# Kernel optimization log

Hardware: AMD Instinct MI355X
Metric: run time of the kernel (lower is better)

## Reference

```python
import jax, jax.numpy as jnp
import numpy as np

B, S, D = 2, 1024, 4096
HQ, HKV, HD = 32, 8, 128
GROUPS = HQ // HKV          # 4
SCALE = HD ** -0.5


def _rope_tables(key):
    # standard RoPE cos/sin tables, non-interleaved (half-split) layout
    inv_freq = 1.0 / (10000.0 ** (jnp.arange(0, HD, 2, dtype=jnp.float32) / HD))  # [HD/2]
    pos = jnp.arange(S, dtype=jnp.float32)                                        # [S]
    freqs = pos[:, None] * inv_freq[None, :]                                      # [S, HD/2]
    emb = jnp.concatenate([freqs, freqs], axis=-1)                                # [S, HD]
    cos = jnp.broadcast_to(jnp.cos(emb)[None], (B, S, HD))
    sin = jnp.broadcast_to(jnp.sin(emb)[None], (B, S, HD))
    return cos, sin


def setup_inputs() -> dict:
    key = jax.random.key(0)
    ks = jax.random.split(key, 6)
    hidden_states = jax.random.normal(ks[0], (B, S, D), dtype=jnp.float32)
    cos_table, sin_table = _rope_tables(ks[1])
    Wq = jax.random.normal(ks[2], (D, HQ * HD), dtype=jnp.float32) * (D ** -0.5)
    Wk = jax.random.normal(ks[3], (D, HKV * HD), dtype=jnp.float32) * (D ** -0.5)
    Wv = jax.random.normal(ks[4], (D, HKV * HD), dtype=jnp.float32) * (D ** -0.5)
    Wo = jax.random.normal(ks[5], (HQ * HD, D), dtype=jnp.float32) * ((HQ * HD) ** -0.5)
    return {"hidden_states": hidden_states, "cos_table": cos_table,
            "sin_table": sin_table, "Wq": Wq, "Wk": Wk, "Wv": Wv, "Wo": Wo}


def _rotate_half(x):
    x1, x2 = jnp.split(x, 2, axis=-1)
    return jnp.concatenate([-x2, x1], axis=-1)


def _apply_rope(x, cos, sin):
    # x: [B, S, H, HD]; cos/sin: [B, S, HD] broadcast across heads
    c = cos[:, :, None, :]
    s = sin[:, :, None, :]
    return x * c + _rotate_half(x) * s


def reference(hidden_states, cos_table, sin_table, Wq, Wk, Wv, Wo):
    b, s, _ = hidden_states.shape
    # QKV projections (no bias, Llama-style)
    q = (hidden_states @ Wq).reshape(b, s, HQ, HD)
    k = (hidden_states @ Wk).reshape(b, s, HKV, HD)
    v = (hidden_states @ Wv).reshape(b, s, HKV, HD)
    # fused RoPE on q and k (in [B, S, H, HD] layout, as in source)
    q = _apply_rope(q, cos_table, sin_table)
    k = _apply_rope(k, cos_table, sin_table)
    # -> [B, H, S, HD]
    q = q.transpose(0, 2, 1, 3)
    k = k.transpose(0, 2, 1, 3)
    v = v.transpose(0, 2, 1, 3)
    # GQA repeat_kv: [B, HKV, S, HD] -> [B, HQ, S, HD]
    k = jnp.repeat(k, GROUPS, axis=1)
    v = jnp.repeat(v, GROUPS, axis=1)
    # SDPA, no mask (source calls sdpa without a mask)
    scores = jnp.einsum('bhqd,bhkd->bhqk', q, k) * SCALE
    attn = jax.nn.softmax(scores, axis=-1)
    out = jnp.einsum('bhqk,bhkd->bhqd', attn, v)
    out = out.transpose(0, 2, 1, 3).reshape(b, s, HQ * HD)
    return out @ Wo
```

## Files before the change

### kernel.cpp

```cpp
#include <hip/hip_runtime.h>

#define B_   2
#define S_   1024
#define D_   4096
#define HQ_  32
#define HKV_ 8
#define HD_  128
#define SCALE_ 0.08838834764831845f

typedef unsigned short u16;
typedef __attribute__((ext_vector_type(8))) short s16x8;
typedef __attribute__((ext_vector_type(4))) short s16x4;
typedef __attribute__((ext_vector_type(4))) float f32x4;

#define MFMA(a,b,c) __builtin_amdgcn_mfma_f32_16x16x32_bf16((a),(b),(c),0,0,0)

__device__ __forceinline__ u16 bf16_rne(float x) {
  unsigned u = __float_as_uint(x);
  u += 0x7fffu + ((u >> 16) & 1u);
  return (u16)(u >> 16);
}
__device__ __forceinline__ float bf16_up(u16 h) {
  return __uint_as_float(((unsigned)h) << 16);
}
__device__ __forceinline__ void split2(float x, u16& h, u16& l) {
  h = bf16_rne(x);
  l = bf16_rne(x - bf16_up(h));
}

__device__ __forceinline__ void cvt_hi_lo(float a, float b, unsigned& hi, unsigned& lo) {
  unsigned h, l;
  asm("v_cvt_pk_bf16_f32 %0, %1, %2" : "=v"(h) : "v"(a), "v"(b));
  float ra = __uint_as_float(h << 16);
  float rb = __uint_as_float(h & 0xffff0000u);
  float la = a - ra, lb = b - rb;
  asm("v_cvt_pk_bf16_f32 %0, %1, %2" : "=v"(l) : "v"(la), "v"(lb));
  hi = h; lo = l;
}
__device__ __forceinline__ void pack8(float4 x, float4 y, uint4& h, uint4& l) {
  unsigned h0,h1,h2,h3,l0,l1,l2,l3;
  cvt_hi_lo(x.x, x.y, h0, l0);
  cvt_hi_lo(x.z, x.w, h1, l1);
  cvt_hi_lo(y.x, y.y, h2, l2);
  cvt_hi_lo(y.z, y.w, h3, l3);
  h = make_uint4(h0,h1,h2,h3); l = make_uint4(l0,l1,l2,l3);
}

typedef const __attribute__((address_space(1))) void* gas_ptr;
typedef __attribute__((address_space(3))) void* las_ptr;
__device__ __forceinline__ void gload_lds16(const void* g, void* l) {
  __builtin_amdgcn_global_load_lds((gas_ptr)g, (las_ptr)l, 16, 0, 0);
}

__global__ __launch_bounds__(256) void frag_b(
    const float* __restrict__ W, u16* __restrict__ dh, u16* __restrict__ dl,
    int N, int n0, int Nc16)
{
  __shared__ float T[32][68];
  const int kt = blockIdx.x, nbk = blockIdx.y;
  const int tid = threadIdx.x;
#pragma unroll
  for (int rep = 0; rep < 2; ++rep) {
    int idx = tid + rep * 256;
    int row = idx >> 4, c4 = (idx & 15) * 4;
    float4 v = *reinterpret_cast<const float4*>(&W[(size_t)(kt*32 + row) * N + n0 + nbk*64 + c4]);
    *reinterpret_cast<float4*>(&T[row][c4]) = v;
  }
  __syncthreads();
  const size_t base = ((size_t)kt * Nc16 + nbk * 4) * 512;
  int c = tid;
  int nt = c >> 6, l = c & 63, kc = l >> 4, r = l & 15;
  u16 hh[8], ll[8];
#pragma unroll
  for (int j = 0; j < 8; ++j) split2(T[kc*8 + j][nt*16 + r], hh[j], ll[j]);
  *reinterpret_cast<s16x8*>(&dh[base + (size_t)c * 8]) =
    (s16x8){(short)hh[0],(short)hh[1],(short)hh[2],(short)hh[3],
            (short)hh[4],(short)hh[5],(short)hh[6],(short)hh[7]};
  *reinterpret_cast<s16x8*>(&dl[base + (size_t)c * 8]) =
    (s16x8){(short)ll[0],(short)ll[1],(short)ll[2],(short)ll[3],
            (short)ll[4],(short)ll[5],(short)ll[6],(short)ll[7]};
}

__global__ __launch_bounds__(256) void frag_kv(
    const float* __restrict__ kb, const float* __restrict__ vb,
    const float* __restrict__ cosT, const float* __restrict__ sinT,
    u16* __restrict__ KFh, u16* __restrict__ KFl,
    u16* __restrict__ VFh, u16* __restrict__ VFl)
{
  __shared__ float T[32][132];
  const int bid  = blockIdx.x;
  const int isV  = bid >> 9;
  const int bkvh = (bid >> 5) & 15;
  const int chnk = bid & 31;
  const int tid  = threadIdx.x;
  const int b    = bkvh >> 3, kvh = bkvh & 7;

  const float* src = isV ? vb : kb;
  {
    int r0 = tid >> 5, c4 = (tid & 31) * 4;
    float sgn = (c4 < 64) ? -1.f : 1.f;
#pragma unroll
    for (int it = 0; it < 4; ++it) {
      int row = r0 + it * 8;
      int srow = chnk*32 + row;
      const float* rp = &src[(((size_t)(b * S_ + srow)) * HKV_ + kvh) * HD_];
      float4 v = *reinterpret_cast<const float4*>(rp + c4);
      if (!isV) {
        float4 p  = *reinterpret_cast<const float4*>(rp + (c4 ^ 64));
        float4 cc = *reinterpret_cast<const float4*>(&cosT[((size_t)(b*S_ + srow))*HD_ + c4]);
        float4 ss = *reinterpret_cast<const float4*>(&sinT[((size_t)(b*S_ + srow))*HD_ + c4]);
        v.x = v.x*cc.x + sgn*p.x*ss.x;
        v.y = v.y*cc.y + sgn*p.y*ss.y;
        v.z = v.z*cc.z + sgn*p.z*ss.z;
// ... 213 lines not shown
  float inv_l[4];
#pragma unroll
  for (int r = 0; r < 4; ++r) inv_l[r] = 1.f / l_run[r];
#pragma unroll
  for (int df = 0; df < 8; ++df)
#pragma unroll
    for (int r = 0; r < 4; ++r) {
      int row = qt * 128 + wid * 16 + lg * 4 + r;
      ob[((size_t)((b * S_ + row) * HQ_ + h)) * HD_ + df*16 + lr] = acc_o[df][r] * inv_l[r];
    }
}

__global__ __launch_bounds__(512) void gemm_p1(
    const float* __restrict__ X, const float* __restrict__ abp,
    const u16* __restrict__ WF,
    float* __restrict__ qb, float* __restrict__ kb, float* __restrict__ vb,
    float* __restrict__ outp, int mode, int col0)
{
  __shared__ __attribute__((aligned(16))) u16 lds[40960];
  u16* ah0 = lds;
  u16* al0 = lds + 4096;
  u16* ah1 = lds + 8192;
  u16* al1 = lds + 12288;
  u16* bh0 = lds + 16384;
  u16* bh1 = lds + 24576;
  u16* blb = lds + 32768;

  const int id   = blockIdx.x;
  const int cpx  = gridDim.x >> 3;
  const int swz  = (id & 7) * cpx + (id >> 3);

  const float* A; const u16* Bh; const u16* Bl; float* C;
  int ldc, Nc16, mb, nb;
  if (mode == 0) {
    if (swz < 128)      { A=X; Bh=WF;          Bl=WF+8388608;  C=qb; ldc=4096; Nc16=128; mb=swz>>3; nb=swz&7; }
    else if (swz < 192) { int u=swz-128; A=X; Bh=WF+16777216; Bl=WF+20971520; C=kb; ldc=1024; Nc16=64; mb=u>>2; nb=u&3; }
    else                { int u=swz-192; A=X; Bh=WF+25165824; Bl=WF+29360128; C=vb; ldc=1024; Nc16=64; mb=u>>2; nb=u&3; }
  } else if (mode == 1) {
    A=X; Bh=WF; Bl=WF+8388608; C=qb+col0; ldc=4096; Nc16=128; mb=swz>>3; nb=swz&7;
  } else if (mode == 2) {
    if (swz < 64) { A=X; Bh=WF;          Bl=WF+4194304;  C=kb; ldc=1024; Nc16=64; mb=swz>>2; nb=swz&3; }
    else          { int u=swz-64; A=X; Bh=WF+8388608; Bl=WF+12582912; C=vb; ldc=1024; Nc16=64; mb=u>>2; nb=u&3; }
  } else if (mode == 3) {
    A=abp; Bh=WF; Bl=WF+16777216; C=outp; ldc=4096; Nc16=256; mb=swz>>4; nb=swz&15;
  } else if (mode == 4) {
    A=abp; Bh=WF; Bl=WF+8388608; C=outp+col0; ldc=4096; Nc16=128; mb=swz>>3; nb=swz&7;
  } else {
    if (swz < 128)      { A=X; Bh=WF;          Bl=WF+8388608;  C=qb;      ldc=4096; Nc16=128; mb=swz>>3; nb=swz&7; }
    else if (swz < 256) { int u=swz-128; A=X; Bh=WF+16777216; Bl=WF+25165824; C=qb+2048; ldc=4096; Nc16=128; mb=u>>3; nb=u&7; }
    else if (swz < 320) { int u=swz-256; A=X; Bh=WF+33554432; Bl=WF+37748736; C=kb; ldc=1024; Nc16=64; mb=u>>2; nb=u&3; }
    else                { int u=swz-320; A=X; Bh=WF+41943040; Bl=WF+46137344; C=vb; ldc=1024; Nc16=64; mb=u>>2; nb=u&3; }
  }

  const int tid  = threadIdx.x;
  const int lane = tid & 63;
  const int wid  = tid >> 6;
  const int mtb  = (wid >> 2) * 4;
  const int ntb  = (wid & 3) * 4;
  const int loff = lane * 8;
  const int lg   = lane >> 4;
  const int lr_  = lane & 15;
  const int aoff = (lg*16 + ((lr_ + 4*lg) & 15)) * 8;

  const int arow = tid >> 2;
  const int akc  = tid & 3;
  const float* aptr = A + (size_t)(mb*128 + arow) * 4096 + akc*8;
  const int awr = (arow >> 4)*512 + (akc*16 + (((arow & 15) + 4*akc) & 15))*8;

  const size_t bStep = (size_t)Nc16 * 512;
  const u16* pBh = Bh + (size_t)nb*16*512 + loff;
  const u16* pBl = Bl + (size_t)nb*16*512 + loff;

  f32x4 acc[4][4];
#pragma unroll
  for (int i = 0; i < 4; ++i)
#pragma unroll
    for (int j = 0; j < 4; ++j) acc[i][j] = (f32x4){0.f, 0.f, 0.f, 0.f};

  float4 ra0 = *reinterpret_cast<const float4*>(aptr);
// ... 43 lines not shown

    s16x8 b_l[4];
#pragma unroll
    for (int nf = 0; nf < 4; ++nf)
      b_l[nf] = *reinterpret_cast<const s16x8*>(&blb[(ntb+nf)*512 + loff]);
#pragma unroll
    for (int mf = 0; mf < 4; ++mf)
#pragma unroll
      for (int nf = 0; nf < 4; ++nf)
        acc[mf][nf] = MFMA(a_h[mf], b_l[nf], acc[mf][nf]);
    if (kt < 127) {
      uint4 h4, l4; pack8(ra0, ra1, h4, l4);
      *reinterpret_cast<uint4*>(&nAh[awr]) = h4;
      *reinterpret_cast<uint4*>(&nAl[awr]) = l4;
      if (kt < 126) {
        ra0 = *reinterpret_cast<const float4*>(aptr + (kt+2)*32);
        ra1 = *reinterpret_cast<const float4*>(aptr + (kt+2)*32 + 4);
      }
    }
    __syncthreads();
  }

  const int row0 = mb*128 + (wid >> 2) * 64;
  const int nloc = nb*256 + (wid & 3) * 64;
#pragma unroll
  for (int mf = 0; mf < 4; ++mf)
#pragma unroll
    for (int nf = 0; nf < 4; ++nf)
#pragma unroll
      for (int r = 0; r < 4; ++r)
        C[(size_t)(row0 + mf*16 + lg*4 + r) * ldc + nloc + nf*16 + lr_] = acc[mf][nf][r];
}

__device__ __forceinline__ void gemm_core_128x256(
    const float* __restrict__ A, const float* __restrict__ W,
    float* __restrict__ C, int ldw, int m0, int n0)
{
  __shared__ u16 Ah[128][40];
  __shared__ u16 Al[128][40];
  __shared__ u16 Bh[256][40];
  __shared__ u16 Bl[256][40];

  const int tid  = threadIdx.x;
  const int lane = tid & 63;
  const int wid  = tid >> 6;
  const int wm   = (wid >> 2) * 64;
  const int wn   = (wid & 3) * 64;
  const int lr   = lane & 15;
  const int lg   = lane >> 4;

  f32x4 acc[4][4];
#pragma unroll
  for (int i = 0; i < 4; ++i)
#pragma unroll
    for (int j = 0; j < 4; ++j) acc[i][j] = (f32x4){0.f, 0.f, 0.f, 0.f};

  const int ar  = tid >> 3;
  const int ak  = (tid & 7) * 4;
  const int bn  = tid & 255;
  const int bk0 = (tid >> 8) * 16;

  for (int kt = 0; kt < D_ / 32; ++kt) {
    const int k0 = kt * 32;
    __syncthreads();
#pragma unroll
    for (int j = 0; j < 2; ++j) {
      int r = ar + 64 * j;
      float4 v = *reinterpret_cast<const float4*>(&A[(size_t)(m0 + r) * D_ + k0 + ak]);
      u16 h0,h1,h2,h3,l0,l1,l2,l3;
      split2(v.x,h0,l0); split2(v.y,h1,l1); split2(v.z,h2,l2); split2(v.w,h3,l3);
      *reinterpret_cast<s16x4*>(&Ah[r][ak]) = (s16x4){(short)h0,(short)h1,(short)h2,(short)h3};
      *reinterpret_cast<s16x4*>(&Al[r][ak]) = (s16x4){(short)l0,(short)l1,(short)l2,(short)l3};
    }
    {
      const float* wp = W + (size_t)(k0 + bk0) * ldw + (n0 + bn);
#pragma unroll
      for (int q = 0; q < 4; ++q) {
        float v0 = wp[(q*4 + 0) * (size_t)ldw];
        float v1 = wp[(q*4 + 1) * (size_t)ldw];
        float v2 = wp[(q*4 + 2) * (size_t)ldw];
        float v3 = wp[(q*4 + 3) * (size_t)ldw];
        u16 h0,h1,h2,h3,l0,l1,l2,l3;
        split2(v0,h0,l0); split2(v1,h1,l1); split2(v2,h2,l2); split2(v3,h3,l3);
        *reinterpret_cast<s16x4*>(&Bh[bn][bk0 + q*4]) = (s16x4){(short)h0,(short)h1,(short)h2,(short)h3};
        *reinterpret_cast<s16x4*>(&Bl[bn][bk0 + q*4]) = (s16x4){(short)l0,(short)l1,(short)l2,(short)l3};
      }
    }
    __syncthreads();
    s16x8 a_h[4], a_l[4], b_h[4], b_l[4];
#pragma unroll
    for (int mf = 0; mf < 4; ++mf) {
      a_h[mf] = *reinterpret_cast<const s16x8*>(&Ah[wm + mf*16 + lr][lg*8]);
      a_l[mf] = *reinterpret_cast<const s16x8*>(&Al[wm + mf*16 + lr][lg*8]);
    }
#pragma unroll
    for (int nf = 0; nf < 4; ++nf) {
      b_h[nf] = *reinterpret_cast<const s16x8*>(&Bh[wn + nf*16 + lr][lg*8]);
      b_l[nf] = *reinterpret_cast<const s16x8*>(&Bl[wn + nf*16 + lr][lg*8]);
    }
#pragma unroll
    for (int mf = 0; mf < 4; ++mf)
#pragma unroll
      for (int nf = 0; nf < 4; ++nf) {
        acc[mf][nf] = MFMA(a_h[mf], b_h[nf], acc[mf][nf]);
        acc[mf][nf] = MFMA(a_l[mf], b_h[nf], acc[mf][nf]);
        acc[mf][nf] = MFMA(a_h[mf], b_l[nf], acc[mf][nf]);
      }
  }
#pragma unroll
  for (int mf = 0; mf < 4; ++mf)
#pragma unroll
    for (int nf = 0; nf < 4; ++nf)
#pragma unroll
      for (int r = 0; r < 4; ++r) {
        int row = m0 + wm + mf*16 + lg*4 + r;
        int col = n0 + wn + nf*16 + lr;
        C[(size_t)row * ldw + col] = acc[mf][nf][r];
      }
}

__global__ __launch_bounds__(512) void gemm_qkv_kernel(
    const float* __restrict__ X,
    const float* __restrict__ Wq, const float* __restrict__ Wk,
    const float* __restrict__ Wv,
    float* __restrict__ qb, float* __restrict__ kb, float* __restrict__ vb)
{
  int nbv = blockIdx.x;
  int m0 = blockIdx.y * 128;
  const float* W; float* C; int ldw, n0;
  if (nbv < 16)      { W = Wq; C = qb; ldw = HQ_*HD_;  n0 = nbv * 256; }
  else if (nbv < 20) { W = Wk; C = kb; ldw = HKV_*HD_; n0 = (nbv-16) * 256; }
  else               { W = Wv; C = vb; ldw = HKV_*HD_; n0 = (nbv-20) * 256; }
  gemm_core_128x256(X, W, C, ldw, m0, n0);
}

__global__ __launch_bounds__(512) void gemm_out_kernel(
    const float* __restrict__ A, const float* __restrict__ Wo, float* __restrict__ out)
{
  gemm_core_128x256(A, Wo, out, D_, blockIdx.y * 128, blockIdx.x * 256);
}

__global__ __launch_bounds__(256) void rope_kernel(
    float* __restrict__ qb, float* __restrict__ kb,
    const float* __restrict__ cosT, const float* __restrict__ sinT)
{
  int idx = blockIdx.x * 256 + threadIdx.x;
  const int nq = B_ * S_ * HQ_ * (HD_/2);
  const int nk = B_ * S_ * HKV_ * (HD_/2);
  if (idx < nq) {
    int j = idx & 63;
    int h = (idx >> 6) & (HQ_ - 1);
    int bs = idx >> 11;
    float* p = qb + ((size_t)bs * HQ_ + h) * HD_;
    const float* cp = cosT + (size_t)bs * HD_;
    const float* sp = sinT + (size_t)bs * HD_;
    float x1 = p[j], x2 = p[j + 64];
    p[j]      = x1 * cp[j]      - x2 * sp[j];
    p[j + 64] = x2 * cp[j + 64] + x1 * sp[j + 64];
  } else if (idx < nq + nk) {
    int t2 = idx - nq;
    int j = t2 & 63;
    int h = (t2 >> 6) & (HKV_ - 1);
    int bs = t2 >> 9;
    float* p = kb + ((size_t)bs * HKV_ + h) * HD_;
    const float* cp = cosT + (size_t)bs * HD_;
    const float* sp = sinT + (size_t)bs * HD_;
    float x1 = p[j], x2 = p[j + 64];
    p[j]      = x1 * cp[j]      - x2 * sp[j];
    p[j + 64] = x2 * cp[j + 64] + x1 * sp[j + 64];
  }
}

__global__ __launch_bounds__(512) void attn_kernel(
    const float* __restrict__ qb, const float* __restrict__ kb,
    const float* __restrict__ vb, float* __restrict__ ob)
{
  __shared__ u16 Kh[64][136], Kl[64][136];
  __shared__ u16 Vh[128][72], Vl[128][72];
  __shared__ u16 Ph[8][16][72], Pl[8][16][72];

  const int tid  = threadIdx.x;
  const int lane = tid & 63;
  const int wid  = tid >> 6;
  const int lr   = lane & 15;
  const int lg   = lane >> 4;
  const int qt   = blockIdx.x;
  const int bh   = blockIdx.y;
  const int b    = bh >> 5, h = bh & 31, kvh = h >> 2;

  s16x8 qh[4], ql[4];
  {
    const int qrow = qt * 128 + wid * 16 + lr;
    const float* qp = qb + ((size_t)((b * S_ + qrow) * HQ_ + h)) * HD_;
#pragma unroll
    for (int kc = 0; kc < 4; ++kc) {
      const float* qp2 = qp + kc * 32 + lg * 8;
      float4 v0 = *reinterpret_cast<const float4*>(qp2);
      float4 v1 = *reinterpret_cast<const float4*>(qp2 + 4);
      u16 hh[8], ll[8];
      split2(v0.x,hh[0],ll[0]); split2(v0.y,hh[1],ll[1]);
      split2(v0.z,hh[2],ll[2]); split2(v0.w,hh[3],ll[3]);
      split2(v1.x,hh[4],ll[4]); split2(v1.y,hh[5],ll[5]);
      split2(v1.z,hh[6],ll[6]); split2(v1.w,hh[7],ll[7]);
      qh[kc] = (s16x8){(short)hh[0],(short)hh[1],(short)hh[2],(short)hh[3],
                       (short)hh[4],(short)hh[5],(short)hh[6],(short)hh[7]};
      ql[kc] = (s16x8){(short)ll[0],(short)ll[1],(short)ll[2],(short)ll[3],
                       (short)ll[4],(short)ll[5],(short)ll[6],(short)ll[7]};
    }
  }

  f32x4 acc_o[8];
#pragma unroll
  for (int df = 0; df < 8; ++df) acc_o[df] = (f32x4){0.f, 0.f, 0.f, 0.f};
  float m_run[4] = {-1e30f, -1e30f, -1e30f, -1e30f};
  float l_run[4] = {0.f, 0.f, 0.f, 0.f};

  const float* kbase = kb + ((size_t)(b * S_) * HKV_ + kvh) * HD_;
  const float* vbase = vb + ((size_t)(b * S_) * HKV_ + kvh) * HD_;

  for (int t = 0; t < S_ / 64; ++t) {
    const int kk0 = t * 64;
    __syncthreads();
#pragma unroll
    for (int j = 0; j < 4; ++j) {
      int idx = tid + 512 * j;
      int kk = idx >> 5, dq = (idx & 31) * 4;
      float4 v = *reinterpret_cast<const float4*>(kbase + (size_t)(kk0 + kk) * (HKV_*HD_) + dq);
      u16 h0,h1,h2,h3,l0,l1,l2,l3;
      split2(v.x,h0,l0); split2(v.y,h1,l1); split2(v.z,h2,l2); split2(v.w,h3,l3);
      *reinterpret_cast<s16x4*>(&Kh[kk][dq]) = (s16x4){(short)h0,(short)h1,(short)h2,(short)h3};
      *reinterpret_cast<s16x4*>(&Kl[kk][dq]) = (s16x4){(short)l0,(short)l1,(short)l2,(short)l3};
    }
    {
      int d = tid & 127;
      int kkb = (tid >> 7) * 16;
      const float* vcol = vbase + d;
#pragma unroll
      for (int jq = 0; jq < 4; ++jq) {
        u16 h4[4], l4[4];
#pragma unroll
        for (int e = 0; e < 4; ++e) {
          float val = vcol[(size_t)(kk0 + kkb + jq*4 + e) * (HKV_*HD_)];
          split2(val, h4[e], l4[e]);
        }
        *reinterpret_cast<s16x4*>(&Vh[d][kkb + jq*4]) = (s16x4){(short)h4[0],(short)h4[1],(short)h4[2],(short)h4[3]};
        *reinterpret_cast<s16x4*>(&Vl[d][kkb + jq*4]) = (s16x4){(short)l4[0],(short)l4[1],(short)l4[2],(short)l4[3]};
      }
    }
    __syncthreads();
    f32x4 accs[4];
#pragma unroll
    for (int nf = 0; nf < 4; ++nf) accs[nf] = (f32x4){0.f, 0.f, 0.f, 0.f};
#pragma unroll
    for (int nf = 0; nf < 4; ++nf) {
      int krow = nf * 16 + lr;
#pragma unroll
      for (int kc = 0; kc < 4; ++kc) {
        s16x8 kh8 = *reinterpret_cast<const s16x8*>(&Kh[krow][kc*32 + lg*8]);
        s16x8 kl8 = *reinterpret_cast<const s16x8*>(&Kl[krow][kc*32 + lg*8]);
        accs[nf] = MFMA(qh[kc], kh8, accs[nf]);
        accs[nf] = MFMA(ql[kc], kh8, accs[nf]);
        accs[nf] = MFMA(qh[kc], kl8, accs[nf]);
      }
    }
#pragma unroll
    for (int nf = 0; nf < 4; ++nf) accs[nf] *= SCALE_;
    float corr[4], rsum[4];
#pragma unroll
    for (int r = 0; r < 4; ++r) {
      float t0 = fmaxf(fmaxf(accs[0][r], accs[1][r]), fmaxf(accs[2][r], accs[3][r]));
      t0 = fmaxf(t0, __shfl_xor(t0, 1));
      t0 = fmaxf(t0, __shfl_xor(t0, 2));
      t0 = fmaxf(t0, __shfl_xor(t0, 4));
      t0 = fmaxf(t0, __shfl_xor(t0, 8));
      float mnew = fmaxf(m_run[r], t0);
      corr[r] = __expf(m_run[r] - mnew);
      m_run[r] = mnew;
      rsum[r] = 0.f;
    }
#pragma unroll
    for (int nf = 0; nf < 4; ++nf)
#pragma unroll
      for (int r = 0; r < 4; ++r) {
        float p = __expf(accs[nf][r] - m_run[r]);
        rsum[r] += p;
        u16 ph, pl;
        split2(p, ph, pl);
        Ph[wid][lg*4 + r][nf*16 + lr] = ph;
        Pl[wid][lg*4 + r][nf*16 + lr] = pl;
      }
#pragma unroll
    for (int r = 0; r < 4; ++r) {
      float s = rsum[r];
      s += __shfl_xor(s, 1); s += __shfl_xor(s, 2);
      s += __shfl_xor(s, 4); s += __shfl_xor(s, 8);
      l_run[r] = l_run[r] * corr[r] + s;
    }
#pragma unroll
    for (int df = 0; df < 8; ++df)
#pragma unroll
      for (int r = 0; r < 4; ++r) acc_o[df][r] *= corr[r];
    s16x8 pa_h[2], pa_l[2];
#pragma unroll
    for (int kc = 0; kc < 2; ++kc) {
      pa_h[kc] = *reinterpret_cast<const s16x8*>(&Ph[wid][lr][kc*32 + lg*8]);
      pa_l[kc] = *reinterpret_cast<const s16x8*>(&Pl[wid][lr][kc*32 + lg*8]);
    }
#pragma unroll
    for (int df = 0; df < 8; ++df) {
      int dcol = df * 16 + lr;
#pragma unroll
      for (int kc = 0; kc < 2; ++kc) {
        s16x8 vh8 = *reinterpret_cast<const s16x8*>(&Vh[dcol][kc*32 + lg*8]);
        s16x8 vl8 = *reinterpret_cast<const s16x8*>(&Vl[dcol][kc*32 + lg*8]);
        acc_o[df] = MFMA(pa_h[kc], vh8, acc_o[df]);
        acc_o[df] = MFMA(pa_l[kc], vh8, acc_o[df]);
        acc_o[df] = MFMA(pa_h[kc], vl8, acc_o[df]);
      }
    }
  }
  float inv_l[4];
#pragma unroll
  for (int r = 0; r < 4; ++r) inv_l[r] = 1.f / l_run[r];
#pragma unroll
  for (int df = 0; df < 8; ++df)
#pragma unroll
    for (int r = 0; r < 4; ++r) {
      int row = qt * 128 + wid * 16 + lg * 4 + r;
      ob[((size_t)((b * S_ + row) * HQ_ + h)) * HD_ + df*16 + lr] = acc_o[df][r] * inv_l[r];
    }
}

extern "C" void kernel_launch(void* const* d_in, const int* in_sizes, int n_in,
                              void* d_out, int out_size, void* d_ws, size_t ws_size,
                              hipStream_t stream)
{
  const float* hs   = (const float*)d_in[0];
  const float* cosT = (const float*)d_in[1];
  const float* sinT = (const float*)d_in[2];
  const float* Wq   = (const float*)d_in[3];
  const float* Wk   = (const float*)d_in[4];
  const float* Wv   = (const float*)d_in[5];
  const float* Wo   = (const float*)d_in[6];
  float* out = (float*)d_out;

  float* qb = (float*)d_ws;
  float* kb = qb + 8388608;
  float* vb = kb + 2097152;
  float* ab = vb + 2097152;
  u16*   WF = (u16*)(ab + 8388608);

  const size_t WS185 = 184549376ULL;
  const size_t WS144 = 150994944ULL;
  const size_t WS112 = 117440512ULL;
  int total = B_*S_*HQ_*(HD_/2) + B_*S_*HKV_*(HD_/2);

  u16* KFh = WF;
  u16* KFl = WF + 2097152;
  u16* VFh = WF + 4194304;
  u16* VFl = WF + 6291456;

  if (ws_size >= WS185) {
    frag_b<<<dim3(128,32), 256, 0, stream>>>(Wq, WF,          WF+8388608,  4096, 0,    128);
    frag_b<<<dim3(128,32), 256, 0, stream>>>(Wq, WF+16777216, WF+25165824, 4096, 2048, 128);
    frag_b<<<dim3(128,16), 256, 0, stream>>>(Wk, WF+33554432, WF+37748736, 1024, 0,    64);
    frag_b<<<dim3(128,16), 256, 0, stream>>>(Wv, WF+41943040, WF+46137344, 1024, 0,    64);
    gemm_p1<<<384, 512, 0, stream>>>(hs, ab, WF, qb, kb, vb, out, 5, 0);
    frag_kv<<<1024, 256, 0, stream>>>(kb, vb, cosT, sinT, KFh, KFl, VFh, VFl);
    attn3<<<dim3(8, 64), 512, 0, stream>>>(qb, cosT, sinT, KFh, KFl, VFh, VFl, ab);
    frag_b<<<dim3(128,64), 256, 0, stream>>>(Wo, WF, WF+16777216, 4096, 0, 256);
    gemm_p1<<<256, 512, 0, stream>>>(hs, ab, WF, qb, kb, vb, out, 3, 0);
  } else if (ws_size >= WS144) {
    frag_b<<<dim3(128,32), 256, 0, stream>>>(Wq, WF,          WF+8388608,  4096, 0,    128);
    frag_b<<<dim3(128,16), 256, 0, stream>>>(Wk, WF+16777216, WF+20971520, 1024, 0,    64);
    frag_b<<<dim3(128,16), 256, 0, stream>>>(Wv, WF+25165824, WF+29360128, 1024, 0,    64);
    gemm_p1<<<256, 512, 0, stream>>>(hs, ab, WF, qb, kb, vb, out, 0, 0);
    frag_b<<<dim3(128,32), 256, 0, stream>>>(Wq, WF,          WF+8388608,  4096, 2048, 128);
    gemm_p1<<<128, 512, 0, stream>>>(hs, ab, WF, qb, kb, vb, out, 1, 2048);
    frag_kv<<<1024, 256, 0, stream>>>(kb, vb, cosT, sinT, KFh, KFl, VFh, VFl);
    attn3<<<dim3(8, 64), 512, 0, stream>>>(qb, cosT, sinT, KFh, KFl, VFh, VFl, ab);
    frag_b<<<dim3(128,64), 256, 0, stream>>>(Wo, WF,          WF+16777216, 4096, 0,    256);
    gemm_p1<<<256, 512, 0, stream>>>(hs, ab, WF, qb, kb, vb, out, 3, 0);
  } else if (ws_size >= WS112) {
    frag_b<<<dim3(128,32), 256, 0, stream>>>(Wq, WF, WF+8388608, 4096, 0, 128);
    gemm_p1<<<128, 512, 0, stream>>>(hs, ab, WF, qb, kb, vb, out, 1, 0);
    frag_b<<<dim3(128,32), 256, 0, stream>>>(Wq, WF, WF+8388608, 4096, 2048, 128);
    gemm_p1<<<128, 512, 0, stream>>>(hs, ab, WF, qb, kb, vb, out, 1, 2048);
    frag_b<<<dim3(128,16), 256, 0, stream>>>(Wk, WF,           WF+4194304,  1024, 0, 64);
    frag_b<<<dim3(128,16), 256, 0, stream>>>(Wv, WF+8388608,   WF+12582912, 1024, 0, 64);
    gemm_p1<<<128, 512, 0, stream>>>(hs, ab, WF, qb, kb, vb, out, 2, 0);
    frag_kv<<<1024, 256, 0, stream>>>(kb, vb, cosT, sinT, KFh, KFl, VFh, VFl);
    attn3<<<dim3(8, 64), 512, 0, stream>>>(qb, cosT, sinT, KFh, KFl, VFh, VFl, ab);
    frag_b<<<dim3(128,32), 256, 0, stream>>>(Wo, WF, WF+8388608, 4096, 0, 128);
    gemm_p1<<<128, 512, 0, stream>>>(hs, ab, WF, qb, kb, vb, out, 4, 0);
    frag_b<<<dim3(128,32), 256, 0, stream>>>(Wo, WF, WF+8388608, 4096, 2048, 128);
    gemm_p1<<<128, 512, 0, stream>>>(hs, ab, WF, qb, kb, vb, out, 4, 2048);
  } else {
    gemm_qkv_kernel<<<dim3(24, 16), 512, 0, stream>>>(hs, Wq, Wk, Wv, qb, kb, vb);
    rope_kernel<<<dim3((total + 255)/256), 256, 0, stream>>>(qb, kb, cosT, sinT);
    attn_kernel<<<dim3(8, 64), 512, 0, stream>>>(qb, kb, vb, ab);
    gemm_out_kernel<<<dim3(16, 16), 512, 0, stream>>>(ab, Wo, out);
  }
}
```

Before: 712.6 us.

## Pre-split activations into bf16 fragments and use 256x256 DMA-staged GEMMs

Adds a frag_a kernel that pre-splits activations (hidden states and attention output) into hi/lo bf16 MFMA fragment layout. New 256x256-tile GEMMs load both operands with global_load_lds double buffering over a 3-pass virtual K loop (hi*hi, lo*hi, hi*lo). The output projection is split-K in two halves, followed by an add kernel. This removes the per-tile fp32-to-bf16 split of A inside the GEMM and increases tile reuse. In exchange it needs a larger workspace, extra passes over memory, and an extra reduction kernel, and it falls back to the old path when the workspace is smaller.

```diff
diff --git a/kernel.cpp b/kernel.cpp
--- a/kernel.cpp
+++ b/kernel.cpp
@@ -52,7 +52,7 @@
   __builtin_amdgcn_global_load_lds((gas_ptr)g, (las_ptr)l, 16, 0, 0);
 }
 
-__global__ __launch_bounds__(256) void frag_b(
+__global__ __launch_bounds__(256) void frag_b1(
     const float* __restrict__ W, u16* __restrict__ dh, u16* __restrict__ dl,
     int N, int n0, int Nc16)
 {
@@ -79,6 +79,188 @@
   *reinterpret_cast<s16x8*>(&dl[base + (size_t)c * 8]) =
     (s16x8){(short)ll[0],(short)ll[1],(short)ll[2],(short)ll[3],
             (short)ll[4],(short)ll[5],(short)ll[6],(short)ll[7]};
+}
+
+__global__ __launch_bounds__(256) void frag_b2(
+    const float* __restrict__ W, u16* __restrict__ dh, u16* __restrict__ dl,
+    int N, int n0, int Nc16)
+{
+  __shared__ float T[32][68];
+  const int kt = blockIdx.x, nbk = blockIdx.y;
+  const int tid = threadIdx.x;
+#pragma unroll
+  for (int rep = 0; rep < 2; ++rep) {
+    int idx = tid + rep * 256;
+    int row = idx >> 4, c4 = (idx & 15) * 4;
+    float4 v = *reinterpret_cast<const float4*>(&W[(size_t)(kt*32 + row) * N + n0 + nbk*64 + c4]);
+    *reinterpret_cast<float4*>(&T[row][c4]) = v;
+  }
+  __syncthreads();
+  int c = tid;
+  int nt = c >> 6, l = c & 63;
+  const size_t base = (((size_t)(kt >> 1) * Nc16 + nbk*4 + nt) * 2 + (kt & 1)) * 512;
+  u16 hh[8], ll[8];
+#pragma unroll
+  for (int j = 0; j < 8; ++j) split2(T[(l >> 4)*8 + j][nt*16 + (l & 15)], hh[j], ll[j]);
+  *reinterpret_cast<s16x8*>(&dh[base + (size_t)l * 8]) =
+    (s16x8){(short)hh[0],(short)hh[1],(short)hh[2],(short)hh[3],
+            (short)hh[4],(short)hh[5],(short)hh[6],(short)hh[7]};
+  *reinterpret_cast<s16x8*>(&dl[base + (size_t)l * 8]) =
+    (s16x8){(short)ll[0],(short)ll[1],(short)ll[2],(short)ll[3],
+            (short)ll[4],(short)ll[5],(short)ll[6],(short)ll[7]};
+}
+
+__global__ __launch_bounds__(256) void frag_a(
+    const float* __restrict__ src, u16* __restrict__ dh, u16* __restrict__ dl)
+{
+  __shared__ float T[128][68];
+  const int kt = blockIdx.x;
+  const int mb = blockIdx.y;
+  const int tid = threadIdx.x;
+#pragma unroll
+  for (int rep = 0; rep < 8; ++rep) {
+    int idx = tid + rep * 256;
+    int row = idx >> 4, c4 = (idx & 15) * 4;
+    float4 v = *reinterpret_cast<const float4*>(&src[(size_t)(mb*128 + row) * 4096 + kt*64 + c4]);
+    *reinterpret_cast<float4*>(&T[row][c4]) = v;
+  }
+  __syncthreads();
+#pragma unroll
+  for (int rep = 0; rep < 4; ++rep) {
+    int c = tid + rep * 256;
+    int mt = c >> 7, rem = c & 127, kk = rem >> 6, l = rem & 63;
+    u16 hh[8], ll[8];
+#pragma unroll
+    for (int j = 0; j < 8; ++j)
+      split2(T[mt*16 + (l & 15)][kk*32 + (l >> 4)*8 + j], hh[j], ll[j]);
+    size_t off = (((size_t)(kt*128 + mb*8 + mt)) * 2 + kk) * 512 + (size_t)l * 8;
+    *reinterpret_cast<s16x8*>(&dh[off]) =
+      (s16x8){(short)hh[0],(short)hh[1],(short)hh[2],(short)hh[3],
+              (short)hh[4],(short)hh[5],(short)hh[6],(short)hh[7]};
+    *reinterpret_cast<s16x8*>(&dl[off]) =
+      (s16x8){(short)ll[0],(short)ll[1],(short)ll[2],(short)ll[3],
+              (short)ll[4],(short)ll[5],(short)ll[6],(short)ll[7]};
+  }
+}
+
+__device__ __forceinline__ void gemm256_core(
+    const u16* __restrict__ PAh, const u16* __restrict__ PAl,
+    const u16* __restrict__ PBh, const u16* __restrict__ PBl,
+    float* __restrict__ C, int ldc, int Nc16,
+    int mb, int nb, int vk0, int nvk, u16* L)
+{
+  const int tid  = threadIdx.x;
+  const int lane = tid & 63;
+  const int wid  = tid >> 6;
+  const int loff = lane * 8;
+  const int wm8  = (wid >> 2) * 8;
+  const int wn4  = (wid & 3) * 4;
+
+  f32x4 acc[8][4];
+#pragma unroll
+  for (int i = 0; i < 8; ++i)
+#pragma unroll
+    for (int j = 0; j < 4; ++j) acc[i][j] = (f32x4){0.f,0.f,0.f,0.f};
+
+  const size_t aBase = (size_t)mb * 16384;
+  const size_t bBase = (size_t)nb * 16384;
+
+#define STAGE256(v, la_, lb_)                                                  \
+  {                                                                            \
+    int p_ = (v) >> 6, vk_ = (v) & 63;                                         \
+    const u16* sa_ = ((p_ == 1) ? PAl : PAh) + (size_t)vk_ * 131072 + aBase;   \
+    const u16* sb_ = ((p_ == 2) ? PBl : PBh) + (size_t)vk_ * ((size_t)Nc16 * 1024) + bBase; \
+    _Pragma("unroll")                                                          \
+    for (int s_ = 0; s_ < 4; ++s_) {                                           \
+      int ch_ = wid * 4 + s_;                                                  \
+      gload_lds16(sa_ + ch_*512 + loff, (la_) + ch_*512);                      \
+      gload_lds16(sb_ + ch_*512 + loff, (lb_) + ch_*512);                      \
+    }                                                                          \
+  }
+
+  {
+    u16* la = L + ((vk0 & 1) ? 16384 : 0);
+    u16* lb = L + 32768 + ((vk0 & 1) ? 16384 : 0);
+    STAGE256(vk0, la, lb);
+  }
+  __syncthreads();
+
+  for (int t = vk0; t < vk0 + nvk; ++t) {
+    u16* la = L + ((t & 1) ? 16384 : 0);
+    u16* lb = L + 32768 + ((t & 1) ? 16384 : 0);
+    if (t + 1 < vk0 + nvk) {
+      u16* na = L + (((t+1) & 1) ? 16384 : 0);
+      u16* nbuf = L + 32768 + (((t+1) & 1) ? 16384 : 0);
+      STAGE256(t+1, na, nbuf);
+    }
+#pragma unroll
+    for (int kk = 0; kk < 2; ++kk) {
+      s16x8 a[8];
+#pragma unroll
+      for (int mf = 0; mf < 8; ++mf)
+        a[mf] = *reinterpret_cast<const s16x8*>(&la[((wm8+mf)*2 + kk)*512 + loff]);
+      __builtin_amdgcn_s_setprio(1);
+#pragma unroll
+      for (int nf = 0; nf < 4; ++nf) {
+        s16x8 b = *reinterpret_cast<const s16x8*>(&lb[((wn4+nf)*2 + kk)*512 + loff]);
+#pragma unroll
+        for (int mf = 0; mf < 8; ++mf)
+          acc[mf][nf] = MFMA(a[mf], b, acc[mf][nf]);
+      }
+      __builtin_amdgcn_s_setprio(0);
+    }
+    __syncthreads();
+  }
+#undef STAGE256
+
+  const int lg = lane >> 4, lr = lane & 15;
+  const int row0 = mb*256 + (wid >> 2) * 128;
+  const int col0 = nb*256 + (wid & 3) * 64;
+#pragma unroll
+  for (int mf = 0; mf < 8; ++mf)
+#pragma unroll
+    for (int nf = 0; nf < 4; ++nf)
+#pragma unroll
+      for (int r = 0; r < 4; ++r)
+        C[(size_t)(row0 + mf*16 + lg*4 + r) * ldc + col0 + nf*16 + lr] = acc[mf][nf][r];
+}
+
+__global__ __launch_bounds__(512) void gemm_qkv2(
+    const u16* __restrict__ XAh, const u16* __restrict__ XAl,
+    const u16* __restrict__ WA,
+    float* __restrict__ qb, float* __restrict__ kb, float* __restrict__ vb)
+{
+  __shared__ __attribute__((aligned(16))) u16 L[65536];
+  int id = blockIdx.x;
+  int swz = (id & 7) * 24 + (id >> 3);
+  const u16 *Bh, *Bl; float* C; int ldc, Nc16, mb, nb;
+  if (swz < 128)      { Bh = WA;          Bl = WA+16777216; C = qb; ldc = 4096; Nc16 = 256; mb = swz & 7;  nb = swz >> 3; }
+  else if (swz < 160) { int u = swz-128; Bh = WA+33554432; Bl = WA+37748736; C = kb; ldc = 1024; Nc16 = 64; mb = u & 7; nb = u >> 3; }
+  else                { int u = swz-160; Bh = WA+41943040; Bl = WA+46137344; C = vb; ldc = 1024; Nc16 = 64; mb = u & 7; nb = u >> 3; }
+  gemm256_core(XAh, XAl, Bh, Bl, C, ldc, Nc16, mb, nb, 0, 192, L);
+}
+
+__global__ __launch_bounds__(512) void gemm_out2(
+    const u16* __restrict__ ABh, const u16* __restrict__ ABl,
+    const u16* __restrict__ WOh, const u16* __restrict__ WOl,
+    float* __restrict__ outp, float* __restrict__ c2)
+{
+  __shared__ __attribute__((aligned(16))) u16 L[65536];
+  int id = blockIdx.x;
+  int swz = (id & 7) * 32 + (id >> 3);
+  int u = swz & 127, s = swz >> 7;
+  int mb = u & 7, nb = u >> 3;
+  gemm256_core(ABh, ABl, WOh, WOl, s ? c2 : outp, 4096, 256, mb, nb, s*96, 96, L);
+}
+
+__global__ __launch_bounds__(256) void add_out(
+    float* __restrict__ o, const float* __restrict__ c2)
+{
+  int i = blockIdx.x * 256 + threadIdx.x;
+  float4 a = reinterpret_cast<float4*>(o)[i];
+  float4 b = reinterpret_cast<const float4*>(c2)[i];
+  a.x += b.x; a.y += b.y; a.z += b.z; a.w += b.w;
+  reinterpret_cast<float4*>(o)[i] = a;
 }
 
 __global__ __launch_bounds__(256) void frag_kv(
@@ -358,19 +540,8 @@
 
   const float* A; const u16* Bh; const u16* Bl; float* C;
   int ldc, Nc16, mb, nb;
-  if (mode == 0) {
-    if (swz < 128)      { A=X; Bh=WF;          Bl=WF+8388608;  C=qb; ldc=4096; Nc16=128; mb=swz>>3; nb=swz&7; }
-    else if (swz < 192) { int u=swz-128; A=X; Bh=WF+16777216; Bl=WF+20971520; C=kb; ldc=1024; Nc16=64; mb=u>>2; nb=u&3; }
-    else                { int u=swz-192; A=X; Bh=WF+25165824; Bl=WF+29360128; C=vb; ldc=1024; Nc16=64; mb=u>>2; nb=u&3; }
-  } else if (mode == 1) {
-    A=X; Bh=WF; Bl=WF+8388608; C=qb+col0; ldc=4096; Nc16=128; mb=swz>>3; nb=swz&7;
-  } else if (mode == 2) {
-    if (swz < 64) { A=X; Bh=WF;          Bl=WF+4194304;  C=kb; ldc=1024; Nc16=64; mb=swz>>2; nb=swz&3; }
-    else          { int u=swz-64; A=X; Bh=WF+8388608; Bl=WF+12582912; C=vb; ldc=1024; Nc16=64; mb=u>>2; nb=u&3; }
-  } else if (mode == 3) {
+  if (mode == 3) {
     A=abp; Bh=WF; Bl=WF+16777216; C=outp; ldc=4096; Nc16=256; mb=swz>>4; nb=swz&15;
-  } else if (mode == 4) {
-    A=abp; Bh=WF; Bl=WF+8388608; C=outp+col0; ldc=4096; Nc16=128; mb=swz>>3; nb=swz&7;
   } else {
     if (swz < 128)      { A=X; Bh=WF;          Bl=WF+8388608;  C=qb;      ldc=4096; Nc16=128; mb=swz>>3; nb=swz&7; }
     else if (swz < 256) { int u=swz-128; A=X; Bh=WF+16777216; Bl=WF+25165824; C=qb+2048; ldc=4096; Nc16=128; mb=u>>3; nb=u&7; }
@@ -480,305 +651,6 @@
         C[(size_t)(row0 + mf*16 + lg*4 + r) * ldc + nloc + nf*16 + lr_] = acc[mf][nf][r];
 }
 
-__device__ __forceinline__ void gemm_core_128x256(
-    const float* __restrict__ A, const float* __restrict__ W,
-    float* __restrict__ C, int ldw, int m0, int n0)
-{
-  __shared__ u16 Ah[128][40];
-  __shared__ u16 Al[128][40];
-  __shared__ u16 Bh[256][40];
-  __shared__ u16 Bl[256][40];
-
-  const int tid  = threadIdx.x;
-  const int lane = tid & 63;
-  const int wid  = tid >> 6;
-  const int wm   = (wid >> 2) * 64;
-  const int wn   = (wid & 3) * 64;
-  const int lr   = lane & 15;
-  const int lg   = lane >> 4;
-
-  f32x4 acc[4][4];
-#pragma unroll
-  for (int i = 0; i < 4; ++i)
-#pragma unroll
-    for (int j = 0; j < 4; ++j) acc[i][j] = (f32x4){0.f, 0.f, 0.f, 0.f};
-
-  const int ar  = tid >> 3;
-  const int ak  = (tid & 7) * 4;
-  const int bn  = tid & 255;
-  const int bk0 = (tid >> 8) * 16;
-
-  for (int kt = 0; kt < D_ / 32; ++kt) {
-    const int k0 = kt * 32;
-    __syncthreads();
-#pragma unroll
-    for (int j = 0; j < 2; ++j) {
-      int r = ar + 64 * j;
-      float4 v = *reinterpret_cast<const float4*>(&A[(size_t)(m0 + r) * D_ + k0 + ak]);
-      u16 h0,h1,h2,h3,l0,l1,l2,l3;
-      split2(v.x,h0,l0); split2(v.y,h1,l1); split2(v.z,h2,l2); split2(v.w,h3,l3);
-      *reinterpret_cast<s16x4*>(&Ah[r][ak]) = (s16x4){(short)h0,(short)h1,(short)h2,(short)h3};
-      *reinterpret_cast<s16x4*>(&Al[r][ak]) = (s16x4){(short)l0,(short)l1,(short)l2,(short)l3};
-    }
-    {
-      const float* wp = W + (size_t)(k0 + bk0) * ldw + (n0 + bn);
-#pragma unroll
-      for (int q = 0; q < 4; ++q) {
-        float v0 = wp[(q*4 + 0) * (size_t)ldw];
-        float v1 = wp[(q*4 + 1) * (size_t)ldw];
-        float v2 = wp[(q*4 + 2) * (size_t)ldw];
-        float v3 = wp[(q*4 + 3) * (size_t)ldw];
-        u16 h0,h1,h2,h3,l0,l1,l2,l3;
-        split2(v0,h0,l0); split2(v1,h1,l1); split2(v2,h2,l2); split2(v3,h3,l3);
-        *reinterpret_cast<s16x4*>(&Bh[bn][bk0 + q*4]) = (s16x4){(short)h0,(short)h1,(short)h2,(short)h3};
-        *reinterpret_cast<s16x4*>(&Bl[bn][bk0 + q*4]) = (s16x4){(short)l0,(short)l1,(short)l2,(short)l3};
-      }
-    }
-    __syncthreads();
-    s16x8 a_h[4], a_l[4], b_h[4], b_l[4];
-#pragma unroll
-    for (int mf = 0; mf < 4; ++mf) {
-      a_h[mf] = *reinterpret_cast<const s16x8*>(&Ah[wm + mf*16 + lr][lg*8]);
-      a_l[mf] = *reinterpret_cast<const s16x8*>(&Al[wm + mf*16 + lr][lg*8]);
-    }
-#pragma unroll
-    for (int nf = 0; nf < 4; ++nf) {
-      b_h[nf] = *reinterpret_cast<const s16x8*>(&Bh[wn + nf*16 + lr][lg*8]);
-      b_l[nf] = *reinterpret_cast<const s16x8*>(&Bl[wn + nf*16 + lr][lg*8]);
-    }
-#pragma unroll
-    for (int mf = 0; mf < 4; ++mf)
-#pragma unroll
-      for (int nf = 0; nf < 4; ++nf) {
-        acc[mf][nf] = MFMA(a_h[mf], b_h[nf], acc[mf][nf]);
-        acc[mf][nf] = MFMA(a_l[mf], b_h[nf], acc[mf][nf]);
-        acc[mf][nf] = MFMA(a_h[mf], b_l[nf], acc[mf][nf]);
-      }
-  }
-#pragma unroll
-  for (int mf = 0; mf < 4; ++mf)
-#pragma unroll
-    for (int nf = 0; nf < 4; ++nf)
-#pragma unroll
-      for (int r = 0; r < 4; ++r) {
-        int row = m0 + wm + mf*16 + lg*4 + r;
-        int col = n0 + wn + nf*16 + lr;
-        C[(size_t)row * ldw + col] = acc[mf][nf][r];
-      }
-}
-
-__global__ __launch_bounds__(512) void gemm_qkv_kernel(
-    const float* __restrict__ X,
-    const float* __restrict__ Wq, const float* __restrict__ Wk,
-    const float* __restrict__ Wv,
-    float* __restrict__ qb, float* __restrict__ kb, float* __restrict__ vb)
-{
-  int nbv = blockIdx.x;
-  int m0 = blockIdx.y * 128;
-  const float* W; float* C; int ldw, n0;
-  if (nbv < 16)      { W = Wq; C = qb; ldw = HQ_*HD_;  n0 = nbv * 256; }
-  else if (nbv < 20) { W = Wk; C = kb; ldw = HKV_*HD_; n0 = (nbv-16) * 256; }
-  else               { W = Wv; C = vb; ldw = HKV_*HD_; n0 = (nbv-20) * 256; }
-  gemm_core_128x256(X, W, C, ldw, m0, n0);
-}
-
-__global__ __launch_bounds__(512) void gemm_out_kernel(
-    const float* __restrict__ A, const float* __restrict__ Wo, float* __restrict__ out)
-{
-  gemm_core_128x256(A, Wo, out, D_, blockIdx.y * 128, blockIdx.x * 256);
-}
-
-__global__ __launch_bounds__(256) void rope_kernel(
-    float* __restrict__ qb, float* __restrict__ kb,
-    const float* __restrict__ cosT, const float* __restrict__ sinT)
-{
-  int idx = blockIdx.x * 256 + threadIdx.x;
-  const int nq = B_ * S_ * HQ_ * (HD_/2);
-  const int nk = B_ * S_ * HKV_ * (HD_/2);
-  if (idx < nq) {
-    int j = idx & 63;
-    int h = (idx >> 6) & (HQ_ - 1);
-    int bs = idx >> 11;
-    float* p = qb + ((size_t)bs * HQ_ + h) * HD_;
-    const float* cp = cosT + (size_t)bs * HD_;
-    const float* sp = sinT + (size_t)bs * HD_;
-    float x1 = p[j], x2 = p[j + 64];
-    p[j]      = x1 * cp[j]      - x2 * sp[j];
-    p[j + 64] = x2 * cp[j + 64] + x1 * sp[j + 64];
-  } else if (idx < nq + nk) {
-    int t2 = idx - nq;
-    int j = t2 & 63;
-    int h = (t2 >> 6) & (HKV_ - 1);
-    int bs = t2 >> 9;
-    float* p = kb + ((size_t)bs * HKV_ + h) * HD_;
-    const float* cp = cosT + (size_t)bs * HD_;
-    const float* sp = sinT + (size_t)bs * HD_;
-    float x1 = p[j], x2 = p[j + 64];
-    p[j]      = x1 * cp[j]      - x2 * sp[j];
-    p[j + 64] = x2 * cp[j + 64] + x1 * sp[j + 64];
-  }
-}
-
-__global__ __launch_bounds__(512) void attn_kernel(
-    const float* __restrict__ qb, const float* __restrict__ kb,
-    const float* __restrict__ vb, float* __restrict__ ob)
-{
-  __shared__ u16 Kh[64][136], Kl[64][136];
-  __shared__ u16 Vh[128][72], Vl[128][72];
-  __shared__ u16 Ph[8][16][72], Pl[8][16][72];
-
-  const int tid  = threadIdx.x;
-  const int lane = tid & 63;
-  const int wid  = tid >> 6;
-  const int lr   = lane & 15;
-  const int lg   = lane >> 4;
-  const int qt   = blockIdx.x;
-  const int bh   = blockIdx.y;
-  const int b    = bh >> 5, h = bh & 31, kvh = h >> 2;
-
-  s16x8 qh[4], ql[4];
-  {
-    const int qrow = qt * 128 + wid * 16 + lr;
-    const float* qp = qb + ((size_t)((b * S_ + qrow) * HQ_ + h)) * HD_;
-#pragma unroll
-    for (int kc = 0; kc < 4; ++kc) {
-      const float* qp2 = qp + kc * 32 + lg * 8;
-      float4 v0 = *reinterpret_cast<const float4*>(qp2);
-      float4 v1 = *reinterpret_cast<const float4*>(qp2 + 4);
-      u16 hh[8], ll[8];
-      split2(v0.x,hh[0],ll[0]); split2(v0.y,hh[1],ll[1]);
-      split2(v0.z,hh[2],ll[2]); split2(v0.w,hh[3],ll[3]);
-      split2(v1.x,hh[4],ll[4]); split2(v1.y,hh[5],ll[5]);
-      split2(v1.z,hh[6],ll[6]); split2(v1.w,hh[7],ll[7]);
-      qh[kc] = (s16x8){(short)hh[0],(short)hh[1],(short)hh[2],(short)hh[3],
-                       (short)hh[4],(short)hh[5],(short)hh[6],(short)hh[7]};
-      ql[kc] = (s16x8){(short)ll[0],(short)ll[1],(short)ll[2],(short)ll[3],
-                       (short)ll[4],(short)ll[5],(short)ll[6],(short)ll[7]};
-    }
-  }
-
-  f32x4 acc_o[8];
-#pragma unroll
-  for (int df = 0; df < 8; ++df) acc_o[df] = (f32x4){0.f, 0.f, 0.f, 0.f};
-  float m_run[4] = {-1e30f, -1e30f, -1e30f, -1e30f};
-  float l_run[4] = {0.f, 0.f, 0.f, 0.f};
-
-  const float* kbase = kb + ((size_t)(b * S_) * HKV_ + kvh) * HD_;
-  const float* vbase = vb + ((size_t)(b * S_) * HKV_ + kvh) * HD_;
-
-  for (int t = 0; t < S_ / 64; ++t) {
-    const int kk0 = t * 64;
-    __syncthreads();
-#pragma unroll
-    for (int j = 0; j < 4; ++j) {
-      int idx = tid + 512 * j;
-      int kk = idx >> 5, dq = (idx & 31) * 4;
-      float4 v = *reinterpret_cast<const float4*>(kbase + (size_t)(kk0 + kk) * (HKV_*HD_) + dq);
-      u16 h0,h1,h2,h3,l0,l1,l2,l3;
-      split2(v.x,h0,l0); split2(v.y,h1,l1); split2(v.z,h2,l2); split2(v.w,h3,l3);
-      *reinterpret_cast<s16x4*>(&Kh[kk][dq]) = (s16x4){(short)h0,(short)h1,(short)h2,(short)h3};
-      *reinterpret_cast<s16x4*>(&Kl[kk][dq]) = (s16x4){(short)l0,(short)l1,(short)l2,(short)l3};
-    }
-    {
-      int d = tid & 127;
-      int kkb = (tid >> 7) * 16;
-      const float* vcol = vbase + d;
-#pragma unroll
-      for (int jq = 0; jq < 4; ++jq) {
-        u16 h4[4], l4[4];
-#pragma unroll
-        for (int e = 0; e < 4; ++e) {
-          float val = vcol[(size_t)(kk0 + kkb + jq*4 + e) * (HKV_*HD_)];
-          split2(val, h4[e], l4[e]);
-        }
-        *reinterpret_cast<s16x4*>(&Vh[d][kkb + jq*4]) = (s16x4){(short)h4[0],(short)h4[1],(short)h4[2],(short)h4[3]};
-        *reinterpret_cast<s16x4*>(&Vl[d][kkb + jq*4]) = (s16x4){(short)l4[0],(short)l4[1],(short)l4[2],(short)l4[3]};
-      }
-    }
-    __syncthreads();
-    f32x4 accs[4];
-#pragma unroll
-    for (int nf = 0; nf < 4; ++nf) accs[nf] = (f32x4){0.f, 0.f, 0.f, 0.f};
-#pragma unroll
-    for (int nf = 0; nf < 4; ++nf) {
-      int krow = nf * 16 + lr;
-#pragma unroll
-      for (int kc = 0; kc < 4; ++kc) {
-        s16x8 kh8 = *reinterpret_cast<const s16x8*>(&Kh[krow][kc*32 + lg*8]);
-        s16x8 kl8 = *reinterpret_cast<const s16x8*>(&Kl[krow][kc*32 + lg*8]);
-        accs[nf] = MFMA(qh[kc], kh8, accs[nf]);
-        accs[nf] = MFMA(ql[kc], kh8, accs[nf]);
-        accs[nf] = MFMA(qh[kc], kl8, accs[nf]);
-      }
-    }
-#pragma unroll
-    for (int nf = 0; nf < 4; ++nf) accs[nf] *= SCALE_;
-    float corr[4], rsum[4];
-#pragma unroll
-    for (int r = 0; r < 4; ++r) {
-      float t0 = fmaxf(fmaxf(accs[0][r], accs[1][r]), fmaxf(accs[2][r], accs[3][r]));
-      t0 = fmaxf(t0, __shfl_xor(t0, 1));
-      t0 = fmaxf(t0, __shfl_xor(t0, 2));
-      t0 = fmaxf(t0, __shfl_xor(t0, 4));
-      t0 = fmaxf(t0, __shfl_xor(t0, 8));
-      float mnew = fmaxf(m_run[r], t0);
-      corr[r] = __expf(m_run[r] - mnew);
-      m_run[r] = mnew;
-      rsum[r] = 0.f;
-    }
-#pragma unroll
-    for (int nf = 0; nf < 4; ++nf)
-#pragma unroll
-      for (int r = 0; r < 4; ++r) {
-        float p = __expf(accs[nf][r] - m_run[r]);
-        rsum[r] += p;
-        u16 ph, pl;
-        split2(p, ph, pl);
-        Ph[wid][lg*4 + r][nf*16 + lr] = ph;
-        Pl[wid][lg*4 + r][nf*16 + lr] = pl;
-      }
-#pragma unroll
-    for (int r = 0; r < 4; ++r) {
-      float s = rsum[r];
-      s += __shfl_xor(s, 1); s += __shfl_xor(s, 2);
-      s += __shfl_xor(s, 4); s += __shfl_xor(s, 8);
-      l_run[r] = l_run[r] * corr[r] + s;
-    }
-#pragma unroll
-    for (int df = 0; df < 8; ++df)
-#pragma unroll
-      for (int r = 0; r < 4; ++r) acc_o[df][r] *= corr[r];
-    s16x8 pa_h[2], pa_l[2];
-#pragma unroll
-    for (int kc = 0; kc < 2; ++kc) {
-      pa_h[kc] = *reinterpret_cast<const s16x8*>(&Ph[wid][lr][kc*32 + lg*8]);
-      pa_l[kc] = *reinterpret_cast<const s16x8*>(&Pl[wid][lr][kc*32 + lg*8]);
-    }
-#pragma unroll
-    for (int df = 0; df < 8; ++df) {
-      int dcol = df * 16 + lr;
-#pragma unroll
-      for (int kc = 0; kc < 2; ++kc) {
-        s16x8 vh8 = *reinterpret_cast<const s16x8*>(&Vh[dcol][kc*32 + lg*8]);
-        s16x8 vl8 = *reinterpret_cast<const s16x8*>(&Vl[dcol][kc*32 + lg*8]);
-        acc_o[df] = MFMA(pa_h[kc], vh8, acc_o[df]);
-        acc_o[df] = MFMA(pa_l[kc], vh8, acc_o[df]);
-        acc_o[df] = MFMA(pa_h[kc], vl8, acc_o[df]);
-      }
-    }
-  }
-  float inv_l[4];
-#pragma unroll
-  for (int r = 0; r < 4; ++r) inv_l[r] = 1.f / l_run[r];
-#pragma unroll
-  for (int df = 0; df < 8; ++df)
-#pragma unroll
-    for (int r = 0; r < 4; ++r) {
-      int row = qt * 128 + wid * 16 + lg * 4 + r;
-      ob[((size_t)((b * S_ + row) * HQ_ + h)) * HD_ + df*16 + lr] = acc_o[df][r] * inv_l[r];
-    }
-}
-
 extern "C" void kernel_launch(void* const* d_in, const int* in_sizes, int n_in,
                               void* d_out, int out_size, void* d_ws, size_t ws_size,
                               hipStream_t stream)
@@ -796,57 +668,42 @@
   float* kb = qb + 8388608;
   float* vb = kb + 2097152;
   float* ab = vb + 2097152;
-  u16*   WF = (u16*)(ab + 8388608);
-
+  u16*   FR = (u16*)(ab + 8388608);
+
+  const size_t WS208 = 218103808ULL;
   const size_t WS185 = 184549376ULL;
-  const size_t WS144 = 150994944ULL;
-  const size_t WS112 = 117440512ULL;
-  int total = B_*S_*HQ_*(HD_/2) + B_*S_*HKV_*(HD_/2);
-
-  u16* KFh = WF;
-  u16* KFl = WF + 2097152;
-  u16* VFh = WF + 4194304;
-  u16* VFl = WF + 6291456;
-
-  if (ws_size >= WS185) {
-    frag_b<<<dim3(128,32), 256, 0, stream>>>(Wq, WF,          WF+8388608,  4096, 0,    128);
-    frag_b<<<dim3(128,32), 256, 0, stream>>>(Wq, WF+16777216, WF+25165824, 4096, 2048, 128);
-    frag_b<<<dim3(128,16), 256, 0, stream>>>(Wk, WF+33554432, WF+37748736, 1024, 0,    64);
-    frag_b<<<dim3(128,16), 256, 0, stream>>>(Wv, WF+41943040, WF+46137344, 1024, 0,    64);
+
+  if (ws_size >= WS208) {
+    u16* XAh = FR;
+    u16* XAl = FR + 8388608;
+    u16* WA  = FR + 16777216;
+    frag_a<<<dim3(64,16), 256, 0, stream>>>(hs, XAh, XAl);
+    frag_b2<<<dim3(128,64), 256, 0, stream>>>(Wq, WA,           WA+16777216, 4096, 0, 256);
+    frag_b2<<<dim3(128,16), 256, 0, stream>>>(Wk, WA+33554432,  WA+37748736, 1024, 0, 64);
+    frag_b2<<<dim3(128,16), 256, 0, stream>>>(Wv, WA+41943040,  WA+46137344, 1024, 0, 64);
+    gemm_qkv2<<<192, 512, 0, stream>>>(XAh, XAl, WA, qb, kb, vb);
+    frag_kv<<<1024, 256, 0, stream>>>(kb, vb, cosT, sinT,
+                                      WA, WA+2097152, WA+4194304, WA+6291456);
+    frag_b2<<<dim3(128,64), 256, 0, stream>>>(Wo, WA+8388608, WA+25165824, 4096, 0, 256);
+    attn3<<<dim3(8, 64), 512, 0, stream>>>(qb, cosT, sinT,
+                                           WA, WA+2097152, WA+4194304, WA+6291456, ab);
+    frag_a<<<dim3(64,16), 256, 0, stream>>>(ab, XAh, XAl);
+    gemm_out2<<<256, 512, 0, stream>>>(XAh, XAl, WA+8388608, WA+25165824, out, qb);
+    add_out<<<8192, 256, 0, stream>>>(out, qb);
+  } else {
+    u16* WF = FR;
+    u16* KFh = WF;
+    u16* KFl = WF + 2097152;
+    u16* VFh = WF + 4194304;
+    u16* VFl = WF + 6291456;
+    frag_b1<<<dim3(128,32), 256, 0, stream>>>(Wq, WF,          WF+8388608,  4096, 0,    128);
+    frag_b1<<<dim3(128,32), 256, 0, stream>>>(Wq, WF+16777216, WF+25165824, 4096, 2048, 128);
+    frag_b1<<<dim3(128,16), 256, 0, stream>>>(Wk, WF+33554432, WF+37748736, 1024, 0,    64);
+    frag_b1<<<dim3(128,16), 256, 0, stream>>>(Wv, WF+41943040, WF+46137344, 1024, 0,    64);
     gemm_p1<<<384, 512, 0, stream>>>(hs, ab, WF, qb, kb, vb, out, 5, 0);
     frag_kv<<<1024, 256, 0, stream>>>(kb, vb, cosT, sinT, KFh, KFl, VFh, VFl);
     attn3<<<dim3(8, 64), 512, 0, stream>>>(qb, cosT, sinT, KFh, KFl, VFh, VFl, ab);
-    frag_b<<<dim3(128,64), 256, 0, stream>>>(Wo, WF, WF+16777216, 4096, 0, 256);
+    frag_b1<<<dim3(128,64), 256, 0, stream>>>(Wo, WF, WF+16777216, 4096, 0, 256);
     gemm_p1<<<256, 512, 0, stream>>>(hs, ab, WF, qb, kb, vb, out, 3, 0);
-  } else if (ws_size >= WS144) {
-    frag_b<<<dim3(128,32), 256, 0, stream>>>(Wq, WF,          WF+8388608,  4096, 0,    128);
-    frag_b<<<dim3(128,16), 256, 0, stream>>>(Wk, WF+16777216, WF+20971520, 1024, 0,    64);
-    frag_b<<<dim3(128,16), 256, 0, stream>>>(Wv, WF+25165824, WF+29360128, 1024, 0,    64);
-    gemm_p1<<<256, 512, 0, stream>>>(hs, ab, WF, qb, kb, vb, out, 0, 0);
-    frag_b<<<dim3(128,32), 256, 0, stream>>>(Wq, WF,          WF+8388608,  4096, 2048, 128);
-    gemm_p1<<<128, 512, 0, stream>>>(hs, ab, WF, qb, kb, vb, out, 1, 2048);
-    frag_kv<<<1024, 256, 0, stream>>>(kb, vb, cosT, sinT, KFh, KFl, VFh, VFl);
-    attn3<<<dim3(8, 64), 512, 0, stream>>>(qb, cosT, sinT, KFh, KFl, VFh, VFl, ab);
-    frag_b<<<dim3(128,64), 256, 0, stream>>>(Wo, WF,          WF+16777216, 4096, 0,    256);
-    gemm_p1<<<256, 512, 0, stream>>>(hs, ab, WF, qb, kb, vb, out, 3, 0);
-  } else if (ws_size >= WS112) {
-    frag_b<<<dim3(128,32), 256, 0, stream>>>(Wq, WF, WF+8388608, 4096, 0, 128);
-    gemm_p1<<<128, 512, 0, stream>>>(hs, ab, WF, qb, kb, vb, out, 1, 0);
-    frag_b<<<dim3(128,32), 256, 0, stream>>>(Wq, WF, WF+8388608, 4096, 2048, 128);
-    gemm_p1<<<128, 512, 0, stream>>>(hs, ab, WF, qb, kb, vb, out, 1, 2048);
-    frag_b<<<dim3(128,16), 256, 0, stream>>>(Wk, WF,           WF+4194304,  1024, 0, 64);
-    frag_b<<<dim3(128,16), 256, 0, stream>>>(Wv, WF+8388608,   WF+12582912, 1024, 0, 64);
-    gemm_p1<<<128, 512, 0, stream>>>(hs, ab, WF, qb, kb, vb, out, 2, 0);
-    frag_kv<<<1024, 256, 0, stream>>>(kb, vb, cosT, sinT, KFh, KFl, VFh, VFl);
-    attn3<<<dim3(8, 64), 512, 0, stream>>>(qb, cosT, sinT, KFh, KFl, VFh, VFl, ab);
-    frag_b<<<dim3(128,32), 256, 0, stream>>>(Wo, WF, WF+8388608, 4096, 0, 128);
-    gemm_p1<<<128, 512, 0, stream>>>(hs, ab, WF, qb, kb, vb, out, 4, 0);
-    frag_b<<<dim3(128,32), 256, 0, stream>>>(Wo, WF, WF+8388608, 4096, 2048, 128);
-    gemm_p1<<<128, 512, 0, stream>>>(hs, ab, WF, qb, kb, vb, out, 4, 2048);
-  } else {
-    gemm_qkv_kernel<<<dim3(24, 16), 512, 0, stream>>>(hs, Wq, Wk, Wv, qb, kb, vb);
-    rope_kernel<<<dim3((total + 255)/256), 256, 0, stream>>>(qb, kb, cosT, sinT);
-    attn_kernel<<<dim3(8, 64), 512, 0, stream>>>(qb, kb, vb, ab);
-    gemm_out_kernel<<<dim3(16, 16), 512, 0, stream>>>(ab, Wo, out);
-  }
-}
+  }
+}
```

New measurement: 698.2 us. 2.0% less time.
